# Kernel optimization log

Hardware: AMD Instinct MI355X
Metric: run time of the kernel (lower is better)

## Reference

```python
import jax, jax.numpy as jnp
import numpy as np
from jax import lax

B, T, E = 256, 128, 768      # batch, seq_len, bert emb dim
HE = 256                     # encoder lstm hidden (per direction)
H = 512                      # decoder hidden = 2*HE
SLOT, INTENT = 120, 64
EMB = SLOT // 3              # 40
V = SLOT + 1                 # 121, bos id = SLOT
DIN = EMB + 2 * H            # 1064 decoder lstm input
NEG = -1e12


def lstm_cell(x, h, c, Wih, Whh, bih, bhh):
    # torch gate order: i, f, g, o
    g = x @ Wih.T + h @ Whh.T + (bih + bhh)
    i, f, gg, o = jnp.split(g, 4, axis=-1)
    c = jax.nn.sigmoid(f) * c + jax.nn.sigmoid(i) * jnp.tanh(gg)
    h = jax.nn.sigmoid(o) * jnp.tanh(c)
    return h, c


def setup_inputs() -> dict:
    key = jax.random.key(0)
    ks = jax.random.split(key, 24)
    s = 0.05
    n = lambda k, shp: jax.random.normal(k, shp, jnp.float32) * s
    return {
        'seq_reps': jax.random.normal(ks[0], (B, T, E), jnp.float32),
        'nwp_index': jax.random.randint(ks[1], (B, T, 1), 0, 2),
        'slot_output_mask': jax.random.randint(ks[2], (B, T), 0, 2).astype(bool),
        'emb_table': jax.random.uniform(ks[3], (V, EMB), jnp.float32, -0.1, 0.1),
        # encoder fwd / bwd LSTM
        'Wf_ih': n(ks[4], (4 * HE, E)), 'Wf_hh': n(ks[5], (4 * HE, HE)),
        'bf_ih': n(ks[6], (4 * HE,)), 'bf_hh': n(ks[7], (4 * HE,)),
        'Wb_ih': n(ks[8], (4 * HE, E)), 'Wb_hh': n(ks[9], (4 * HE, HE)),
        'bb_ih': n(ks[10], (4 * HE,)), 'bb_hh': n(ks[11], (4 * HE,)),
        # decoder LSTM
        'Wd_ih': n(ks[12], (4 * H, DIN)), 'Wd_hh': n(ks[13], (4 * H, H)),
        'bd_ih': n(ks[14], (4 * H,)), 'bd_hh': n(ks[15], (4 * H,)),
        # attention + output heads
        'attn_W': n(ks[16], (H, H)), 'attn_b': n(ks[17], (H,)),
        'slot_W': n(ks[18], (SLOT, 2 * H)), 'slot_b': n(ks[19], (SLOT,)),
        'intent_W': n(ks[20], (INTENT, 2 * H)), 'intent_b': n(ks[21], (INTENT,)),
    }


def forward(seq_reps, nwp_index, slot_output_mask, emb_table,
            Wf_ih, Wf_hh, bf_ih, bf_hh, Wb_ih, Wb_hh, bb_ih, bb_hh,
            Wd_ih, Wd_hh, bd_ih, bd_hh, attn_W, attn_b,
            slot_W, slot_b, intent_W, intent_b):
    # ---------- Encoder: 1-layer bidirectional LSTM ----------
    xs = seq_reps.transpose(1, 0, 2)  # [T,B,E]
    z = jnp.zeros((B, HE), seq_reps.dtype)

    def fstep(carry, x):
        h, c = lstm_cell(x, carry[0], carry[1], Wf_ih, Wf_hh, bf_ih, bf_hh)
        return (h, c), h

    def bstep(carry, x):
        h, c = lstm_cell(x, carry[0], carry[1], Wb_ih, Wb_hh, bb_ih, bb_hh)
        return (h, c), h

    _, hf = lax.scan(fstep, (z, z), xs)
    _, hb = lax.scan(bstep, (z, z), xs[::-1])
    enc = jnp.concatenate([hf, hb[::-1]], -1).transpose(1, 0, 2)  # [B,T,512]

    # last real hidden: out[b, #nonzero(nwp_index[b])]
    count = jnp.clip((nwp_index[:, :, 0] != 0).sum(1), 0, T - 1)
    last_hidden = enc[jnp.arange(B), count]  # [B,H]

    # ---------- Attention (energies independent of step -> precompute) ----------
    energies = enc @ attn_W.T + attn_b  # [B,T,H]

    def attention(h):  # h: [B,H]
        e = jnp.einsum('bth,bh->bt', energies, h)
        e = jnp.where(slot_output_mask, NEG, e)
        alpha = jax.nn.softmax(e, -1)
        return jnp.einsum('bt,bth->bh', alpha, enc)  # [B,H]

    # ---------- Decoder: per-timestep LSTM + attention ----------
    bos_emb = jnp.broadcast_to(emb_table[SLOT], (B, EMB))
    zH = jnp.zeros((B, H), seq_reps.dtype)
    aligns = enc.transpose(1, 0, 2)  # [T,B,H]

    def dstep(carry, aligned):
        emb, ctx, h, c = carry
        inp = jnp.concatenate([emb, ctx, aligned], -1)  # [B,1064]
        h, c = lstm_cell(inp, h, c, Wd_ih, Wd_hh, bd_ih, bd_hh)
        score = jnp.concatenate([h, ctx], -1) @ slot_W.T + slot_b
        logp = jax.nn.log_softmax(score, -1)
        nxt = jnp.argmax(logp, -1)
        emb = emb_table[nxt]
        ctx_new = attention(h)
        return (emb, ctx_new, h, c), (logp, h, ctx_new)

    _, (logps, h_seq, ctx_seq) = lax.scan(dstep, (bos_emb, last_hidden, zH, zH), aligns)

    slot_scores = logps.transpose(1, 0, 2)  # [B,T,SLOT]
    # intent computed at step 0: intent_context == attention(h after step 0) == ctx_seq[0]
    intent_score = jnp.concatenate([h_seq[0], ctx_seq[0]], -1) @ intent_W.T + intent_b
    return slot_scores, intent_score


def reference(seq_reps, nwp_index, slot_output_mask, emb_table,
              Wf_ih, Wf_hh, bf_ih, bf_hh, Wb_ih, Wb_hh, bb_ih, bb_hh,
              Wd_ih, Wd_hh, bd_ih, bd_hh, attn_W, attn_b,
              slot_W, slot_b, intent_W, intent_b):
    return forward(seq_reps, nwp_index, slot_output_mask, emb_table,
                   Wf_ih, Wf_hh, bf_ih, bf_hh, Wb_ih, Wb_hh, bb_ih, bb_hh,
                   Wd_ih, Wd_hh, bd_ih, bd_hh, attn_W, attn_b,
                   slot_W, slot_b, intent_W, intent_b)
```

## Files before the change

kernel.cpp:

```cpp
#include <hip/hip_runtime.h>
#include <math.h>

#define Bn 256
#define Tn 128
#define En 768
#define HEn 256
#define Hn 512
#define SLOTn 120
#define INTENTn 64
#define EMBn 40
#define NEGV -1e12f

__device__ __forceinline__ float sigm(float x) { return 1.0f / (1.0f + expf(-x)); }

__global__ void zero_k(float* __restrict__ p, int n) {
    int i = blockIdx.x * blockDim.x + threadIdx.x;
    int stride = gridDim.x * blockDim.x;
    for (; i < n; i += stride) p[i] = 0.f;
}

__global__ void detect_mask_k(const unsigned char* __restrict__ m, int* __restrict__ flag) {
    __shared__ int any;
    if (threadIdx.x == 0) any = 0;
    __syncthreads();
    int found = 0;
    for (int i = threadIdx.x; i < 32768; i += 256) {
        if ((i & 3) != 0 && m[i] != 0) found = 1;
    }
    if (found) atomicOr(&any, 1);
    __syncthreads();
    if (threadIdx.x == 0) *flag = any;
}

__global__ __launch_bounds__(256) void enc_step_k(
    const float* __restrict__ seq,
    const float* __restrict__ Wf_ih, const float* __restrict__ Wf_hh,
    const float* __restrict__ bf_ih, const float* __restrict__ bf_hh,
    const float* __restrict__ Wb_ih, const float* __restrict__ Wb_hh,
    const float* __restrict__ bb_ih, const float* __restrict__ bb_hh,
    const float* __restrict__ hf_in, float* __restrict__ hf_out, float* __restrict__ cf,
    const float* __restrict__ hb_in, float* __restrict__ hb_out, float* __restrict__ cb,
    float* __restrict__ enc, int step)
{
    const int dir = blockIdx.z;
    const float* Wih = dir ? Wb_ih : Wf_ih;
    const float* Whh = dir ? Wb_hh : Wf_hh;
    const float* bih = dir ? bb_ih : bf_ih;
    const float* bhh = dir ? bb_hh : bf_hh;
    const float* h_in = dir ? hb_in : hf_in;
    float* h_out = dir ? hb_out : hf_out;
    float* c_st  = dir ? cb : cf;
    const int t_eff = dir ? (Tn - 1 - step) : step;
    const int nb = blockIdx.x;
    const int b0 = blockIdx.y << 5;
    const int tid = threadIdx.x;
    const int tx = tid & 15, ty = tid >> 4;

    __shared__ float As[32][36];
    __shared__ float Bs[32][68];
    __shared__ float Gs[32][68];

    float acc[2][4] = {};

    for (int kt = 0; kt < 32; ++kt) {
        const int k0 = kt << 5;
#pragma unroll
        for (int r = 0; r < 4; ++r) {
            int idx = tid + (r << 8);
            int kk = idx & 31, row = idx >> 5;
            int k = k0 + kk, b = b0 + row;
            As[kk][row] = (k < En) ? seq[((size_t)b * Tn + t_eff) * En + k]
                                   : h_in[(b << 8) + (k - En)];
        }
#pragma unroll
        for (int r = 0; r < 8; ++r) {
            int idx = tid + (r << 8);
            int kk = idx & 31, c = idx >> 5;
            int j = ((c >> 4) << 8) + (nb << 4) + (c & 15);
            int k = k0 + kk;
            Bs[kk][c] = (k < En) ? Wih[j * En + k] : Whh[(j << 8) + (k - En)];
        }
        __syncthreads();
#pragma unroll
        for (int kk = 0; kk < 32; ++kk) {
            float a0 = As[kk][ty * 2], a1 = As[kk][ty * 2 + 1];
            float w0 = Bs[kk][tx * 4], w1 = Bs[kk][tx * 4 + 1];
            float w2 = Bs[kk][tx * 4 + 2], w3 = Bs[kk][tx * 4 + 3];
            acc[0][0] += a0 * w0; acc[0][1] += a0 * w1; acc[0][2] += a0 * w2; acc[0][3] += a0 * w3;
            acc[1][0] += a1 * w0; acc[1][1] += a1 * w1; acc[1][2] += a1 * w2; acc[1][3] += a1 * w3;
        }
        __syncthreads();
    }

#pragma unroll
    for (int i = 0; i < 2; ++i)
#pragma unroll
        for (int q = 0; q < 4; ++q)
            Gs[ty * 2 + i][tx * 4 + q] = acc[i][q];
    __syncthreads();

#pragma unroll
    for (int r = 0; r < 2; ++r) {
        int p = tid + (r << 8);
        int row = p >> 4, jl = p & 15;
        int jg = (nb << 4) + jl;
        int b = b0 + row;
        float gi = Gs[row][jl]      + bih[jg]           + bhh[jg];
        float gf = Gs[row][16 + jl] + bih[HEn + jg]     + bhh[HEn + jg];
        float gg = Gs[row][32 + jl] + bih[2 * HEn + jg] + bhh[2 * HEn + jg];
        float go = Gs[row][48 + jl] + bih[3 * HEn + jg] + bhh[3 * HEn + jg];
        float ii = sigm(gi), ff = sigm(gf), tg = tanhf(gg), oo = sigm(go);
        int ci = (b << 8) + jg;
        float cn = ff * c_st[ci] + ii * tg;
        float hn = oo * tanhf(cn);
        c_st[ci] = cn;
        h_out[ci] = hn;
        enc[((size_t)t_eff * Bn + b) * Hn + dir * HEn + jg] = hn;
    }
}

__global__ __launch_bounds__(256) void energT_k(
    const float* __restrict__ enc, const float* __restrict__ attn_W,
    float* __restrict__ energT)
{
    const int nb = blockIdx.x;
    const int mb = blockIdx.y;
    const int t = mb >> 2, b0 = (mb & 3) << 6;
    const int tid = threadIdx.x;
    const int tx = tid & 15, ty = tid >> 4;
    __shared__ float As[32][68];
    __shared__ float Bs[32][68];
    float acc[4][4] = {};
    for (int kt = 0; kt < 16; ++kt) {
        int k0 = kt << 5;
#pragma unroll
        for (int r = 0; r < 8; ++r) {
            int idx = tid + (r << 8);
            int kk = idx & 31, row = idx >> 5;
            As[kk][row] = enc[((size_t)t * Bn + b0 + row) * Hn + k0 + kk];
            Bs[kk][row] = attn_W[(nb * 64 + row) * Hn + k0 + kk];
        }
        __syncthreads();
#pragma unroll
        for (int kk = 0; kk < 32; ++kk) {
            float a0 = As[kk][ty * 4], a1 = As[kk][ty * 4 + 1];
            float a2 = As[kk][ty * 4 + 2], a3 = As[kk][ty * 4 + 3];
            float w0 = Bs[kk][tx * 4], w1 = Bs[kk][tx * 4 + 1];
            float w2 = Bs[kk][tx * 4 + 2], w3 = Bs[kk][tx * 4 + 3];
            acc[0][0] += a0 * w0; acc[0][1] += a0 * w1; acc[0][2] += a0 * w2; acc[0][3] += a0 * w3;
            acc[1][0] += a1 * w0; acc[1][1] += a1 * w1; acc[1][2] += a1 * w2; acc[1][3] += a1 * w3;
            acc[2][0] += a2 * w0; acc[2][1] += a2 * w1; acc[2][2] += a2 * w2; acc[2][3] += a2 * w3;
            acc[3][0] += a3 * w0; acc[3][1] += a3 * w1; acc[3][2] += a3 * w2; acc[3][3] += a3 * w3;
        }
        __syncthreads();
    }
#pragma unroll
    for (int i = 0; i < 4; ++i)
#pragma unroll
        for (int q = 0; q < 4; ++q)
            energT[((size_t)(b0 + ty * 4 + i) * Hn + nb * 64 + tx * 4 + q) * Tn + t] = acc[i][q];
}

__global__ __launch_bounds__(64) void init2_k(
    const int* __restrict__ nwp, const float* __restrict__ enc,
    const float* __restrict__ emb_table,
    float* __restrict__ ctx0, float* __restrict__ embb)
{
    int b = blockIdx.x;
    int lane = threadIdx.x;
    int p1 = (nwp[b * Tn + lane] != 0);
    int p2 = (nwp[b * Tn + lane + 64] != 0);
    unsigned long long m1 = __ballot(p1), m2 = __ballot(p2);
    int cnt = __popcll(m1) + __popcll(m2);
    int idx = cnt < (Tn - 1) ? cnt : (Tn - 1);
#pragma unroll
    for (int r = 0; r < 8; ++r) {
        int j = lane + (r << 6);
        ctx0[(b << 9) + j] = enc[((size_t)idx * Bn + b) * Hn + j];
    }
    if (lane < EMBn) embb[b * EMBn + lane] = emb_table[SLOTn * EMBn + lane];
}

__global__ __launch_bounds__(256) void dec_step_k(
    const float* __restrict__ embb, const float* __restrict__ ctx_in,
    const float* __restrict__ enc, const float* __restrict__ h_in,
    float* __restrict__ h_out, float* __restrict__ c_st,
    const float* __restrict__ Wih, const float* __restrict__ Whh,
    const float* __restrict__ bih, const float* __restrict__ bhh,
    float* __restrict__ h0_out, int step)
{
    const int nb = blockIdx.x;
    const int b0 = blockIdx.y << 5;
    const int tid = threadIdx.x;
    const int tx = tid & 15, ty = tid >> 4;

    __shared__ float As[32][36];
    __shared__ float Bs[32][68];
    __shared__ float Gs[32][68];

    float acc[2][4] = {};

    for (int kt = 0; kt < 50; ++kt) {
        const int k0 = kt << 5;
#pragma unroll
        for (int r = 0; r < 4; ++r) {
            int idx = tid + (r << 8);
            int kk = idx & 31, row = idx >> 5;
            int k = k0 + kk, b = b0 + row;
            float v = 0.f;
            if (k < 40) v = embb[b * EMBn + k];
            else if (k < 552) v = ctx_in[(b << 9) + (k - 40)];
            else if (k < 1064) v = enc[((size_t)step * Bn + b) * Hn + (k - 552)];
            else if (k < 1576) v = h_in[(b << 9) + (k - 1064)];
            As[kk][row] = v;
        }
#pragma unroll
        for (int r = 0; r < 8; ++r) {
            int idx = tid + (r << 8);
            int kk = idx & 31, c = idx >> 5;
            int j = ((c >> 4) << 9) + (nb << 4) + (c & 15);
            int k = k0 + kk;
            float w = 0.f;
            if (k < 1064) w = Wih[(size_t)j * 1064 + k];
            else if (k < 1576) w = Whh[(j << 9) + (k - 1064)];
            Bs[kk][c] = w;
        }
        __syncthreads();
#pragma unroll
        for (int kk = 0; kk < 32; ++kk) {
            float a0 = As[kk][ty * 2], a1 = As[kk][ty * 2 + 1];
            float w0 = Bs[kk][tx * 4], w1 = Bs[kk][tx * 4 + 1];
            float w2 = Bs[kk][tx * 4 + 2], w3 = Bs[kk][tx * 4 + 3];
            acc[0][0] += a0 * w0; acc[0][1] += a0 * w1; acc[0][2] += a0 * w2; acc[0][3] += a0 * w3;
            acc[1][0] += a1 * w0; acc[1][1] += a1 * w1; acc[1][2] += a1 * w2; acc[1][3] += a1 * w3;
        }
        __syncthreads();
    }

#pragma unroll
    for (int i = 0; i < 2; ++i)
#pragma unroll
        for (int q = 0; q < 4; ++q)
            Gs[ty * 2 + i][tx * 4 + q] = acc[i][q];
    __syncthreads();

#pragma unroll
    for (int r = 0; r < 2; ++r) {
        int p = tid + (r << 8);
        int row = p >> 4, jl = p & 15;
        int jg = (nb << 4) + jl;
        int b = b0 + row;
        float gi = Gs[row][jl]      + bih[jg]          + bhh[jg];
        float gf = Gs[row][16 + jl] + bih[Hn + jg]     + bhh[Hn + jg];
        float gg = Gs[row][32 + jl] + bih[2 * Hn + jg] + bhh[2 * Hn + jg];
        float go = Gs[row][48 + jl] + bih[3 * Hn + jg] + bhh[3 * Hn + jg];
        float ii = sigm(gi), ff = sigm(gf), tg = tanhf(gg), oo = sigm(go);
        int ci = (b << 9) + jg;
        float cn = ff * c_st[ci] + ii * tg;
        float hn = oo * tanhf(cn);
        c_st[ci] = cn;
        h_out[ci] = hn;
        if (h0_out) h0_out[ci] = hn;
    }
}

__global__ __launch_bounds__(256) void dec_attn_slot_k(
    const float* __restrict__ enc, const float* __restrict__ energT,
    const float* __restrict__ h, const float* __restrict__ ctx_in,
    float* __restrict__ ctx_out, const unsigned char* __restrict__ mask_u8,
    const int* __restrict__ mask_i32, const int* __restrict__ mask_flag,
    const float* __restrict__ slot_W, const float* __restrict__ slot_b,
    const float* __restrict__ emb_table, float* __restrict__ embb,
    float* __restrict__ out_slot, float* __restrict__ ctx0_save, int step)
{
    __shared__ float hs[512];
    __shared__ float red[256];
    __shared__ float es[128];
    __shared__ float ins[8][1032];
    __shared__ float Ws[16][132];
    __shared__ float sc[8][132];
    __shared__ float logZ[8];
    __shared__ int amax[8];

    const int bid = blockIdx.x;
    const int tid = threadIdx.x;

    if (bid < Bn) {
        const int b = bid;
        hs[tid] = h[(b << 9) + tid];
        hs[tid + 256] = h[(b << 9) + 256 + tid];
        __syncthreads();
        const int tp = tid & 127, half = tid >> 7;
        const float* ept = energT + ((size_t)b * Hn + (half << 8)) * Tn + tp;
        const float* hp = hs + (half << 8);
        float acc = 0.f;
#pragma unroll 8
        for (int j = 0; j < 256; ++j) acc += ept[(size_t)j * Tn] * hp[j];
        red[tid] = acc;
        __syncthreads();
        if (tid < 128) {
            float e = red[tid] + red[tid + 128];
            bool mv = (*mask_flag) ? (mask_u8[(size_t)b * Tn + tid] != 0)
                                   : (mask_i32[(size_t)b * Tn + tid] != 0);
            if (mv) e = NEGV;
            es[tid] = e;
        }
        __syncthreads();
        if (tid < 64) {
            float v = fmaxf(es[tid], es[tid + 64]);
            for (int o = 32; o; o >>= 1) v = fmaxf(v, __shfl_down(v, o));
            if (tid == 0) red[0] = v;
        }
        __syncthreads();
        float m = red[0];
        if (tid < 128) es[tid] = __expf(es[tid] - m);
        __syncthreads();
        if (tid < 64) {
            float v = es[tid] + es[tid + 64];
            for (int o = 32; o; o >>= 1) v += __shfl_down(v, o);
            if (tid == 0) red[0] = v;
        }
        __syncthreads();
        float inv = 1.0f / red[0];
        if (tid < 128) es[tid] *= inv;
        __syncthreads();
        float c0 = 0.f, c1 = 0.f;
        const float* ep = enc + (b << 9) + tid;
#pragma unroll 4
        for (int t2 = 0; t2 < Tn; ++t2) {
            float a = es[t2];
            c0 += a * ep[(size_t)t2 * Bn * Hn];
            c1 += a * ep[(size_t)t2 * Bn * Hn + 256];
        }
        ctx_out[(b << 9) + tid] = c0;
        ctx_out[(b << 9) + tid + 256] = c1;
        if (ctx0_save) {
            ctx0_save[(b << 9) + tid] = c0;
            ctx0_save[(b << 9) + tid + 256] = c1;
        }
    } else {
        const int b_base = (bid - Bn) << 3;
        for (int r = 0; r < 32; ++r) {
            int idx = tid + (r << 8);
            int bl = idx >> 10, k = idx & 1023;
            int b = b_base + bl;
            ins[bl][k] = (k < 512) ? h[(b << 9) + k] : ctx_in[(b << 9) + (k - 512)];
        }
        __syncthreads();
        const int s = tid & 127, bh = tid >> 7;
        float acc[4] = {};
        for (int kt = 0; kt < 64; ++kt) {
            int k0 = kt << 4;
#pragma unroll
            for (int r = 0; r < 8; ++r) {
                int idx = tid + (r << 8);
                int kk = idx & 15, ss = idx >> 4;
                Ws[kk][ss] = (ss < SLOTn) ? slot_W[ss * 1024 + k0 + kk] : 0.f;
            }
            __syncthreads();
#pragma unroll
            for (int kk = 0; kk < 16; ++kk) {
                float w = Ws[kk][s];
#pragma unroll
                for (int i = 0; i < 4; ++i) acc[i] += w * ins[(bh << 2) + i][k0 + kk];
            }
            __syncthreads();
        }
        if (s < SLOTn) {
#pragma unroll
            for (int i = 0; i < 4; ++i) sc[(bh << 2) + i][s] = acc[i] + slot_b[s];
        }
        __syncthreads();
        if (tid < 8) {
            float mm = -INFINITY; int am = 0;
            for (int ss = 0; ss < SLOTn; ++ss) {
                float v = sc[tid][ss];
                if (v > mm) { mm = v; am = ss; }
            }
            float sum = 0.f;
            for (int ss = 0; ss < SLOTn; ++ss) sum += __expf(sc[tid][ss] - mm);
            logZ[tid] = mm + logf(sum);
            amax[tid] = am;
        }
        __syncthreads();
        for (int r = 0; r < 4; ++r) {
            int idx = tid + (r << 8);
            int bl = idx >> 7, ss = idx & 127;
            if (ss < SLOTn)
                out_slot[(size_t)(b_base + bl) * Tn * SLOTn + step * SLOTn + ss] =
                    sc[bl][ss] - logZ[bl];
        }
        for (int i = tid; i < 8 * EMBn; i += 256) {
            int bl = i / EMBn, e2 = i % EMBn;
            embb[(b_base + bl) * EMBn + e2] = emb_table[amax[bl] * EMBn + e2];
        }
    }
}

__global__ __launch_bounds__(256) void intent_k(
    const float* __restrict__ h0, const float* __restrict__ ctx0,
    const float* __restrict__ W, const float* __restrict__ bias,
    float* __restrict__ out)
{
    __shared__ float ins[8][1032];
    __shared__ float Ws[16][68];
    const int tid = threadIdx.x;
    const int b_base = blockIdx.x << 3;
    for (int r = 0; r < 32; ++r) {
        int idx = tid + (r << 8);
        int bl = idx >> 10, k = idx & 1023;
        int b = b_base + bl;
        ins[bl][k] = (k < 512) ? h0[(b << 9) + k] : ctx0[(b << 9) + (k - 512)];
    }
    __syncthreads();
    const int n = tid & 63, bq = tid >> 6;
    float acc0 = 0.f, acc1 = 0.f;
    for (int kt = 0; kt < 64; ++kt) {
        int k0 = kt << 4;
#pragma unroll
        for (int r = 0; r < 4; ++r) {
            int idx = tid + (r << 8);
            int kk = idx & 15, nn = idx >> 4;
            Ws[kk][nn] = W[nn * 1024 + k0 + kk];
        }
        __syncthreads();
#pragma unroll
        for (int kk = 0; kk < 16; ++kk) {
            float w = Ws[kk][n];
            acc0 += w * ins[bq * 2][k0 + kk];
            acc1 += w * ins[bq * 2 + 1][k0 + kk];
        }
        __syncthreads();
    }
    out[(b_base + bq * 2) * INTENTn + n] = acc0 + bias[n];
    out[(b_base + bq * 2 + 1) * INTENTn + n] = acc1 + bias[n];
}

extern "C" void kernel_launch(void* const* d_in, const int* in_sizes, int n_in,
                              void* d_out, int out_size, void* d_ws, size_t ws_size,
                              hipStream_t stream) {
    (void)in_sizes; (void)n_in; (void)out_size; (void)ws_size;

    const float* seq      = (const float*)d_in[0];
    const int*   nwp      = (const int*)d_in[1];
    const unsigned char* mask_u8 = (const unsigned char*)d_in[2];
    const int*   mask_i32 = (const int*)d_in[2];
    const float* embt     = (const float*)d_in[3];
    const float* Wf_ih    = (const float*)d_in[4];
    const float* Wf_hh    = (const float*)d_in[5];
    const float* bf_ih    = (const float*)d_in[6];
    const float* bf_hh    = (const float*)d_in[7];
    const float* Wb_ih    = (const float*)d_in[8];
    const float* Wb_hh    = (const float*)d_in[9];
    const float* bb_ih    = (const float*)d_in[10];
    const float* bb_hh    = (const float*)d_in[11];
    const float* Wd_ih    = (const float*)d_in[12];
    const float* Wd_hh    = (const float*)d_in[13];
    const float* bd_ih    = (const float*)d_in[14];
    const float* bd_hh    = (const float*)d_in[15];
    const float* attn_W   = (const float*)d_in[16];
    const float* slot_W   = (const float*)d_in[18];
    const float* slot_b   = (const float*)d_in[19];
    const float* intent_W = (const float*)d_in[20];
    const float* intent_b = (const float*)d_in[21];

    float* Wp = (float*)d_ws;
    size_t off = 0;
    float* enc    = Wp + off; off += (size_t)Tn * Bn * Hn;
    float* energT = Wp + off; off += (size_t)Bn * Hn * Tn;
    float* zbase  = Wp + off;
    float* hf0 = Wp + off; off += Bn * HEn;
    float* hf1 = Wp + off; off += Bn * HEn;
    float* cf  = Wp + off; off += Bn * HEn;
    float* hb0 = Wp + off; off += Bn * HEn;
    float* hb1 = Wp + off; off += Bn * HEn;
    float* cb  = Wp + off; off += Bn * HEn;
    float* hd0 = Wp + off; off += Bn * Hn;
    float* hd1 = Wp + off; off += Bn * Hn;
    float* cd  = Wp + off; off += Bn * Hn;
    int nzero = (int)(Wp + off - zbase);
    float* ctx0b = Wp + off; off += Bn * Hn;
    float* ctx1b = Wp + off; off += Bn * Hn;
    float* h0s   = Wp + off; off += Bn * Hn;
    float* ctx0s = Wp + off; off += Bn * Hn;
    float* embb  = Wp + off; off += Bn * EMBn;
    int* mask_flag = (int*)(Wp + off); off += 1;

    float* out = (float*)d_out;

    zero_k<<<512, 256, 0, stream>>>(zbase, nzero);
    detect_mask_k<<<1, 256, 0, stream>>>(mask_u8, mask_flag);

    for (int s = 0; s < Tn; ++s) {
        const float* hinf = (s & 1) ? hf1 : hf0;
        float* houtf      = (s & 1) ? hf0 : hf1;
        const float* hinb = (s & 1) ? hb1 : hb0;
        float* houtb      = (s & 1) ? hb0 : hb1;
        enc_step_k<<<dim3(16, 8, 2), 256, 0, stream>>>(
            seq, Wf_ih, Wf_hh, bf_ih, bf_hh, Wb_ih, Wb_hh, bb_ih, bb_hh,
            hinf, houtf, cf, hinb, houtb, cb, enc, s);
    }

    energT_k<<<dim3(8, 512), 256, 0, stream>>>(enc, attn_W, energT);
    init2_k<<<256, 64, 0, stream>>>(nwp, enc, embt, ctx0b, embb);

    for (int t = 0; t < Tn; ++t) {
        const float* ctxin = (t & 1) ? ctx1b : ctx0b;
        float* ctxout      = (t & 1) ? ctx0b : ctx1b;
        const float* hin   = (t & 1) ? hd1 : hd0;
        float* hout        = (t & 1) ? hd0 : hd1;
        dec_step_k<<<dim3(32, 8), 256, 0, stream>>>(
            embb, ctxin, enc, hin, hout, cd,
            Wd_ih, Wd_hh, bd_ih, bd_hh, (t == 0) ? h0s : (float*)nullptr, t);
        dec_attn_slot_k<<<288, 256, 0, stream>>>(
            enc, energT, hout, ctxin, ctxout, mask_u8, mask_i32, mask_flag,
            slot_W, slot_b, embt, embb, out, (t == 0) ? ctx0s : (float*)nullptr, t);
    }

    intent_k<<<32, 256, 0, stream>>>(h0s, ctx0s, intent_W, intent_b,
                                     out + (size_t)Bn * Tn * SLOTn);
}
```

Measured before the change: 46.25 ms.

## Restructure LSTM step GEMMs, attention reductions and slot projection with float4 loads

Encoder and decoder step kernels drop the shared-memory activation tile. Each wavefront now reads activations directly from global memory as float4 and dots them against a weight tile in LDS, with the next weight tile prefetched into registers. The attention energy and context reductions switch to float4 loads with a different split across threads. The slot projection reads a pre-transposed, float4-packed copy of slot_W built once at startup. The goal is fewer barriers and more vectorised memory traffic, at the cost of uncoalesced, redundant global activation reads across the 64 lanes that rely on cache hits.

```diff
diff --git a/kernel.cpp b/kernel.cpp
--- a/kernel.cpp
+++ b/kernel.cpp
@@ -30,6 +30,23 @@
     if (found) atomicOr(&any, 1);
     __syncthreads();
     if (threadIdx.x == 0) *flag = any;
+}
+
+__global__ __launch_bounds__(256) void slotwt_k(const float* __restrict__ W,
+                                               float* __restrict__ wT4) {
+    int idx = blockIdx.x * 256 + threadIdx.x;
+    int k = idx >> 7, s = idx & 127;
+    float v = (s < SLOTn) ? W[(size_t)s * 1024 + k] : 0.f;
+    wT4[((size_t)(k >> 2) * 128 + s) * 4 + (k & 3)] = v;
+}
+
+__device__ __forceinline__ float4 f4zero() { float4 z; z.x = z.y = z.z = z.w = 0.f; return z; }
+
+__device__ __forceinline__ float4 enc_wload(const float* __restrict__ Wih,
+                                            const float* __restrict__ Whh,
+                                            int jrow, int k) {
+    return (k < En) ? *(const float4*)(Wih + (size_t)jrow * En + k)
+                    : *(const float4*)(Whh + (size_t)jrow * HEn + (k - En));
 }
 
 __global__ __launch_bounds__(256) void enc_step_k(
@@ -43,67 +60,69 @@
     float* __restrict__ enc, int step)
 {
     const int dir = blockIdx.z;
-    const float* Wih = dir ? Wb_ih : Wf_ih;
-    const float* Whh = dir ? Wb_hh : Wf_hh;
-    const float* bih = dir ? bb_ih : bf_ih;
-    const float* bhh = dir ? bb_hh : bf_hh;
-    const float* h_in = dir ? hb_in : hf_in;
-    float* h_out = dir ? hb_out : hf_out;
-    float* c_st  = dir ? cb : cf;
+    const float* __restrict__ Wih = dir ? Wb_ih : Wf_ih;
+    const float* __restrict__ Whh = dir ? Wb_hh : Wf_hh;
+    const float* __restrict__ bih = dir ? bb_ih : bf_ih;
+    const float* __restrict__ bhh = dir ? bb_hh : bf_hh;
+    const float* __restrict__ h_in = dir ? hb_in : hf_in;
+    float* __restrict__ h_out = dir ? hb_out : hf_out;
+    float* __restrict__ c_st  = dir ? cb : cf;
     const int t_eff = dir ? (Tn - 1 - step) : step;
-    const int nb = blockIdx.x;
+
+    const int jb = blockIdx.x;
     const int b0 = blockIdx.y << 5;
     const int tid = threadIdx.x;
-    const int tx = tid & 15, ty = tid >> 4;
-
-    __shared__ float As[32][36];
-    __shared__ float Bs[32][68];
+    const int c   = tid & 63;
+    const int wid = __builtin_amdgcn_readfirstlane(tid >> 6);
+    const int bw  = b0 + (wid << 3);
+
+    __shared__ float Bs[64][44];
     __shared__ float Gs[32][68];
 
-    float acc[2][4] = {};
+    const int c0_ = tid >> 3,          kq0 = tid & 7;
+    const int c1_ = (tid + 256) >> 3,  kq1 = tid & 7;
+    const int j0row = ((c0_ >> 4) << 8) + (jb << 4) + (c0_ & 15);
+    const int j1row = ((c1_ >> 4) << 8) + (jb << 4) + (c1_ & 15);
+
+    float acc[8] = {0,0,0,0,0,0,0,0};
+    float4 r0 = enc_wload(Wih, Whh, j0row, kq0 * 4);
+    float4 r1 = enc_wload(Wih, Whh, j1row, kq1 * 4);
 
     for (int kt = 0; kt < 32; ++kt) {
         const int k0 = kt << 5;
-#pragma unroll
-        for (int r = 0; r < 4; ++r) {
-            int idx = tid + (r << 8);
-            int kk = idx & 31, row = idx >> 5;
-            int k = k0 + kk, b = b0 + row;
-            As[kk][row] = (k < En) ? seq[((size_t)b * Tn + t_eff) * En + k]
-                                   : h_in[(b << 8) + (k - En)];
-        }
-#pragma unroll
-        for (int r = 0; r < 8; ++r) {
-            int idx = tid + (r << 8);
-            int kk = idx & 31, c = idx >> 5;
-            int j = ((c >> 4) << 8) + (nb << 4) + (c & 15);
-            int k = k0 + kk;
-            Bs[kk][c] = (k < En) ? Wih[j * En + k] : Whh[(j << 8) + (k - En)];
-        }
-        __syncthreads();
-#pragma unroll
-        for (int kk = 0; kk < 32; ++kk) {
-            float a0 = As[kk][ty * 2], a1 = As[kk][ty * 2 + 1];
-            float w0 = Bs[kk][tx * 4], w1 = Bs[kk][tx * 4 + 1];
-            float w2 = Bs[kk][tx * 4 + 2], w3 = Bs[kk][tx * 4 + 3];
-            acc[0][0] += a0 * w0; acc[0][1] += a0 * w1; acc[0][2] += a0 * w2; acc[0][3] += a0 * w3;
-            acc[1][0] += a1 * w0; acc[1][1] += a1 * w1; acc[1][2] += a1 * w2; acc[1][3] += a1 * w3;
-        }
-        __syncthreads();
-    }
-
-#pragma unroll
-    for (int i = 0; i < 2; ++i)
-#pragma unroll
-        for (int q = 0; q < 4; ++q)
-            Gs[ty * 2 + i][tx * 4 + q] = acc[i][q];
+        __syncthreads();
+        *(float4*)&Bs[c0_][kq0 * 4] = r0;
+        *(float4*)&Bs[c1_][kq1 * 4] = r1;
+        __syncthreads();
+        if (kt < 31) {
+            r0 = enc_wload(Wih, Whh, j0row, k0 + 32 + kq0 * 4);
+            r1 = enc_wload(Wih, Whh, j1row, k0 + 32 + kq1 * 4);
+        }
+#pragma unroll
+        for (int g = 0; g < 8; ++g) {
+            const int kk = k0 + (g << 2);
+            const float* __restrict__ abase;
+            size_t astr;
+            if (kk < En) { abase = seq + ((size_t)bw * Tn + t_eff) * En + kk; astr = (size_t)Tn * En; }
+            else         { abase = h_in + ((size_t)bw << 8) + (kk - En);      astr = HEn; }
+            float4 bf = *(const float4*)&Bs[c][g << 2];
+#pragma unroll
+            for (int i = 0; i < 8; ++i) {
+                float4 a = *(const float4*)(abase + (size_t)i * astr);
+                acc[i] += a.x * bf.x + a.y * bf.y + a.z * bf.z + a.w * bf.w;
+            }
+        }
+    }
+
+#pragma unroll
+    for (int i = 0; i < 8; ++i) Gs[(wid << 3) + i][c] = acc[i];
     __syncthreads();
 
 #pragma unroll
     for (int r = 0; r < 2; ++r) {
         int p = tid + (r << 8);
         int row = p >> 4, jl = p & 15;
-        int jg = (nb << 4) + jl;
+        int jg = (jb << 4) + jl;
         int b = b0 + row;
         float gi = Gs[row][jl]      + bih[jg]           + bhh[jg];
         float gf = Gs[row][16 + jl] + bih[HEn + jg]     + bhh[HEn + jg];
@@ -181,6 +200,14 @@
     if (lane < EMBn) embb[b * EMBn + lane] = emb_table[SLOTn * EMBn + lane];
 }
 
+__device__ __forceinline__ float4 dec_wload(const float* __restrict__ Wih,
+                                            const float* __restrict__ Whh,
+                                            int jrow, int k) {
+    if (k < 1064) return *(const float4*)(Wih + (size_t)jrow * 1064 + k);
+    if (k < 1576) return *(const float4*)(Whh + ((size_t)jrow << 9) + (k - 1064));
+    return f4zero();
+}
+
 __global__ __launch_bounds__(256) void dec_step_k(
     const float* __restrict__ embb, const float* __restrict__ ctx_in,
     const float* __restrict__ enc, const float* __restrict__ h_in,
@@ -189,66 +216,64 @@
     const float* __restrict__ bih, const float* __restrict__ bhh,
     float* __restrict__ h0_out, int step)
 {
-    const int nb = blockIdx.x;
+    const int jb = blockIdx.x;
     const int b0 = blockIdx.y << 5;
     const int tid = threadIdx.x;
-    const int tx = tid & 15, ty = tid >> 4;
-
-    __shared__ float As[32][36];
-    __shared__ float Bs[32][68];
+    const int c   = tid & 63;
+    const int wid = __builtin_amdgcn_readfirstlane(tid >> 6);
+    const int bw  = b0 + (wid << 3);
+
+    __shared__ float Bs[64][44];
     __shared__ float Gs[32][68];
 
-    float acc[2][4] = {};
+    const int c0_ = tid >> 3,          kq0 = tid & 7;
+    const int c1_ = (tid + 256) >> 3,  kq1 = tid & 7;
+    const int j0row = ((c0_ >> 4) << 9) + (jb << 4) + (c0_ & 15);
+    const int j1row = ((c1_ >> 4) << 9) + (jb << 4) + (c1_ & 15);
+
+    float acc[8] = {0,0,0,0,0,0,0,0};
+    float4 r0 = dec_wload(Wih, Whh, j0row, kq0 * 4);
+    float4 r1 = dec_wload(Wih, Whh, j1row, kq1 * 4);
 
     for (int kt = 0; kt < 50; ++kt) {
         const int k0 = kt << 5;
-#pragma unroll
-        for (int r = 0; r < 4; ++r) {
-            int idx = tid + (r << 8);
-            int kk = idx & 31, row = idx >> 5;
-            int k = k0 + kk, b = b0 + row;
-            float v = 0.f;
-            if (k < 40) v = embb[b * EMBn + k];
-            else if (k < 552) v = ctx_in[(b << 9) + (k - 40)];
-            else if (k < 1064) v = enc[((size_t)step * Bn + b) * Hn + (k - 552)];
-            else if (k < 1576) v = h_in[(b << 9) + (k - 1064)];
-            As[kk][row] = v;
-        }
-#pragma unroll
-        for (int r = 0; r < 8; ++r) {
-            int idx = tid + (r << 8);
-            int kk = idx & 31, c = idx >> 5;
-            int j = ((c >> 4) << 9) + (nb << 4) + (c & 15);
-            int k = k0 + kk;
-            float w = 0.f;
-            if (k < 1064) w = Wih[(size_t)j * 1064 + k];
-            else if (k < 1576) w = Whh[(j << 9) + (k - 1064)];
-            Bs[kk][c] = w;
-        }
-        __syncthreads();
-#pragma unroll
-        for (int kk = 0; kk < 32; ++kk) {
-            float a0 = As[kk][ty * 2], a1 = As[kk][ty * 2 + 1];
-            float w0 = Bs[kk][tx * 4], w1 = Bs[kk][tx * 4 + 1];
-            float w2 = Bs[kk][tx * 4 + 2], w3 = Bs[kk][tx * 4 + 3];
-            acc[0][0] += a0 * w0; acc[0][1] += a0 * w1; acc[0][2] += a0 * w2; acc[0][3] += a0 * w3;
-            acc[1][0] += a1 * w0; acc[1][1] += a1 * w1; acc[1][2] += a1 * w2; acc[1][3] += a1 * w3;
-        }
-        __syncthreads();
-    }
-
-#pragma unroll
-    for (int i = 0; i < 2; ++i)
-#pragma unroll
-        for (int q = 0; q < 4; ++q)
-            Gs[ty * 2 + i][tx * 4 + q] = acc[i][q];
+        __syncthreads();
+        *(float4*)&Bs[c0_][kq0 * 4] = r0;
+        *(float4*)&Bs[c1_][kq1 * 4] = r1;
+        __syncthreads();
+        if (kt < 49) {
+            r0 = dec_wload(Wih, Whh, j0row, k0 + 32 + kq0 * 4);
+            r1 = dec_wload(Wih, Whh, j1row, k0 + 32 + kq1 * 4);
+        }
+#pragma unroll
+        for (int g = 0; g < 8; ++g) {
+            const int kk = k0 + (g << 2);
+            if (kk < 1576) {
+                const float* __restrict__ abase;
+                size_t astr;
+                if (kk < 40)        { abase = embb   + (size_t)bw * EMBn + kk;               astr = EMBn; }
+                else if (kk < 552)  { abase = ctx_in + ((size_t)bw << 9) + (kk - 40);        astr = Hn; }
+                else if (kk < 1064) { abase = enc + ((size_t)step * Bn + bw) * Hn + (kk - 552); astr = Hn; }
+                else                { abase = h_in  + ((size_t)bw << 9) + (kk - 1064);       astr = Hn; }
+                float4 bf = *(const float4*)&Bs[c][g << 2];
+#pragma unroll
+                for (int i = 0; i < 8; ++i) {
+                    float4 a = *(const float4*)(abase + (size_t)i * astr);
+                    acc[i] += a.x * bf.x + a.y * bf.y + a.z * bf.z + a.w * bf.w;
+                }
+            }
+        }
+    }
+
+#pragma unroll
+    for (int i = 0; i < 8; ++i) Gs[(wid << 3) + i][c] = acc[i];
     __syncthreads();
 
 #pragma unroll
     for (int r = 0; r < 2; ++r) {
         int p = tid + (r << 8);
         int row = p >> 4, jl = p & 15;
-        int jg = (nb << 4) + jl;
+        int jg = (jb << 4) + jl;
         int b = b0 + row;
         float gi = Gs[row][jl]      + bih[jg]          + bhh[jg];
         float gf = Gs[row][16 + jl] + bih[Hn + jg]     + bhh[Hn + jg];
@@ -269,15 +294,16 @@
     const float* __restrict__ h, const float* __restrict__ ctx_in,
     float* __restrict__ ctx_out, const unsigned char* __restrict__ mask_u8,
     const int* __restrict__ mask_i32, const int* __restrict__ mask_flag,
-    const float* __restrict__ slot_W, const float* __restrict__ slot_b,
+    const float* __restrict__ wT4, const float* __restrict__ slot_b,
     const float* __restrict__ emb_table, float* __restrict__ embb,
     float* __restrict__ out_slot, float* __restrict__ ctx0_save, int step)
 {
     __shared__ float hs[512];
-    __shared__ float red[256];
+    __shared__ float red2[8][132];
     __shared__ float es[128];
-    __shared__ float ins[8][1032];
-    __shared__ float Ws[16][132];
+    __shared__ float redm[2];
+    __shared__ float ctxp[2][512];
+    __shared__ float pacc[2][8][132];
     __shared__ float sc[8][132];
     __shared__ float logZ[8];
     __shared__ int amax[8];
@@ -290,85 +316,95 @@
         hs[tid] = h[(b << 9) + tid];
         hs[tid + 256] = h[(b << 9) + 256 + tid];
         __syncthreads();
-        const int tp = tid & 127, half = tid >> 7;
-        const float* ept = energT + ((size_t)b * Hn + (half << 8)) * Tn + tp;
-        const float* hp = hs + (half << 8);
-        float acc = 0.f;
+        {
+            const int tg = tid & 31, jg = tid >> 5;
+            const float* __restrict__ ep = energT + ((size_t)b * Hn + jg * 64) * Tn + (tg << 2);
+            float4 a = f4zero();
 #pragma unroll 8
-        for (int j = 0; j < 256; ++j) acc += ept[(size_t)j * Tn] * hp[j];
-        red[tid] = acc;
+            for (int jj = 0; jj < 64; ++jj) {
+                float hv = hs[jg * 64 + jj];
+                float4 e4 = *(const float4*)(ep + (size_t)jj * Tn);
+                a.x += e4.x * hv; a.y += e4.y * hv; a.z += e4.z * hv; a.w += e4.w * hv;
+            }
+            *(float4*)&red2[jg][tg << 2] = a;
+        }
         __syncthreads();
         if (tid < 128) {
-            float e = red[tid] + red[tid + 128];
+            float e = 0.f;
+#pragma unroll
+            for (int jg = 0; jg < 8; ++jg) e += red2[jg][tid];
             bool mv = (*mask_flag) ? (mask_u8[(size_t)b * Tn + tid] != 0)
                                    : (mask_i32[(size_t)b * Tn + tid] != 0);
-            if (mv) e = NEGV;
-            es[tid] = e;
+            es[tid] = mv ? NEGV : e;
         }
         __syncthreads();
         if (tid < 64) {
             float v = fmaxf(es[tid], es[tid + 64]);
             for (int o = 32; o; o >>= 1) v = fmaxf(v, __shfl_down(v, o));
-            if (tid == 0) red[0] = v;
-        }
-        __syncthreads();
-        float m = red[0];
+            if (tid == 0) redm[0] = v;
+        }
+        __syncthreads();
+        float m = redm[0];
         if (tid < 128) es[tid] = __expf(es[tid] - m);
         __syncthreads();
         if (tid < 64) {
             float v = es[tid] + es[tid + 64];
             for (int o = 32; o; o >>= 1) v += __shfl_down(v, o);
-            if (tid == 0) red[0] = v;
-        }
-        __syncthreads();
-        float inv = 1.0f / red[0];
+            if (tid == 0) redm[0] = v;
+        }
+        __syncthreads();
+        float inv = 1.0f / redm[0];
         if (tid < 128) es[tid] *= inv;
         __syncthreads();
-        float c0 = 0.f, c1 = 0.f;
-        const float* ep = enc + (b << 9) + tid;
-#pragma unroll 4
-        for (int t2 = 0; t2 < Tn; ++t2) {
-            float a = es[t2];
-            c0 += a * ep[(size_t)t2 * Bn * Hn];
-            c1 += a * ep[(size_t)t2 * Bn * Hn + 256];
-        }
-        ctx_out[(b << 9) + tid] = c0;
-        ctx_out[(b << 9) + tid + 256] = c1;
-        if (ctx0_save) {
-            ctx0_save[(b << 9) + tid] = c0;
-            ctx0_save[(b << 9) + tid + 256] = c1;
+        {
+            const int dq = tid & 127, th = tid >> 7;
+            const int d = dq << 2;
+            const float* __restrict__ ep2 = enc + (b << 9) + d;
+            float4 a = f4zero();
+            const int tbase = th << 6;
+#pragma unroll 8
+            for (int t2 = 0; t2 < 64; ++t2) {
+                float al = es[tbase + t2];
+                float4 e4 = *(const float4*)(ep2 + (size_t)(tbase + t2) * (Bn * Hn));
+                a.x += al * e4.x; a.y += al * e4.y; a.z += al * e4.z; a.w += al * e4.w;
+            }
+            *(float4*)&ctxp[th][d] = a;
+        }
+        __syncthreads();
+        {
+            float v0 = ctxp[0][tid] + ctxp[1][tid];
+            float v1 = ctxp[0][tid + 256] + ctxp[1][tid + 256];
+            ctx_out[(b << 9) + tid] = v0;
+            ctx_out[(b << 9) + 256 + tid] = v1;
+            if (ctx0_save) {
+                ctx0_save[(b << 9) + tid] = v0;
+                ctx0_save[(b << 9) + 256 + tid] = v1;
+            }
         }
     } else {
         const int b_base = (bid - Bn) << 3;
-        for (int r = 0; r < 32; ++r) {
-            int idx = tid + (r << 8);
-            int bl = idx >> 10, k = idx & 1023;
-            int b = b_base + bl;
-            ins[bl][k] = (k < 512) ? h[(b << 9) + k] : ctx_in[(b << 9) + (k - 512)];
-        }
-        __syncthreads();
-        const int s = tid & 127, bh = tid >> 7;
-        float acc[4] = {};
-        for (int kt = 0; kt < 64; ++kt) {
-            int k0 = kt << 4;
-#pragma unroll
-            for (int r = 0; r < 8; ++r) {
-                int idx = tid + (r << 8);
-                int kk = idx & 15, ss = idx >> 4;
-                Ws[kk][ss] = (ss < SLOTn) ? slot_W[ss * 1024 + k0 + kk] : 0.f;
-            }
-            __syncthreads();
-#pragma unroll
-            for (int kk = 0; kk < 16; ++kk) {
-                float w = Ws[kk][s];
-#pragma unroll
-                for (int i = 0; i < 4; ++i) acc[i] += w * ins[(bh << 2) + i][k0 + kk];
-            }
-            __syncthreads();
-        }
-        if (s < SLOTn) {
-#pragma unroll
-            for (int i = 0; i < 4; ++i) sc[(bh << 2) + i][s] = acc[i] + slot_b[s];
+        const int sl = tid & 127;
+        const int kg = __builtin_amdgcn_readfirstlane(tid >> 7);
+        const float* __restrict__ a0 = (kg ? ctx_in : h) + ((size_t)b_base << 9);
+        const float* __restrict__ wb = wT4 + (size_t)kg * 128 * 128 * 4;
+        float acc[8] = {0,0,0,0,0,0,0,0};
+        for (int k4 = 0; k4 < 128; ++k4) {
+            const int k = k4 << 2;
+            float4 w4 = *(const float4*)(wb + ((size_t)k4 * 128 + sl) * 4);
+#pragma unroll
+            for (int i = 0; i < 8; ++i) {
+                const float* __restrict__ ar = a0 + ((size_t)i << 9) + k;
+                acc[i] += w4.x * ar[0] + w4.y * ar[1] + w4.z * ar[2] + w4.w * ar[3];
+            }
+        }
+#pragma unroll
+        for (int i = 0; i < 8; ++i) pacc[kg][i][sl] = acc[i];
+        __syncthreads();
+        if (tid < 128) {
+            float sb = (tid < SLOTn) ? slot_b[tid] : 0.f;
+#pragma unroll
+            for (int i = 0; i < 8; ++i)
+                sc[i][tid] = pacc[0][i][tid] + pacc[1][i][tid] + sb;
         }
         __syncthreads();
         if (tid < 8) {
@@ -485,11 +521,13 @@
     float* ctx0s = Wp + off; off += Bn * Hn;
     float* embb  = Wp + off; off += Bn * EMBn;
     int* mask_flag = (int*)(Wp + off); off += 1;
+    float* wT4   = Wp + off; off += 1024 * 128;
 
     float* out = (float*)d_out;
 
     zero_k<<<512, 256, 0, stream>>>(zbase, nzero);
     detect_mask_k<<<1, 256, 0, stream>>>(mask_u8, mask_flag);
+    slotwt_k<<<512, 256, 0, stream>>>(slot_W, wT4);
 
     for (int s = 0; s < Tn; ++s) {
         const float* hinf = (s & 1) ? hf1 : hf0;
@@ -514,7 +552,7 @@
             Wd_ih, Wd_hh, bd_ih, bd_hh, (t == 0) ? h0s : (float*)nullptr, t);
         dec_attn_slot_k<<<288, 256, 0, stream>>>(
             enc, energT, hout, ctxin, ctxout, mask_u8, mask_i32, mask_flag,
-            slot_W, slot_b, embt, embb, out, (t == 0) ? ctx0s : (float*)nullptr, t);
+            wT4, slot_b, embt, embb, out, (t == 0) ? ctx0s : (float*)nullptr, t);
     }
 
     intent_k<<<32, 256, 0, stream>>>(h0s, ctx0s, intent_W, intent_b,
```

After: 47.51 ms. +2.7%, slower.
